# Kernel optimization log

Measured on AMD Instinct MI355X. Metric: run time of the kernel, lower is better.

## Reference

```python
import jax, jax.numpy as jnp
import numpy as np

FACTOR = 5

def setup_inputs() -> dict:
    key = jax.random.key(0)
    k1, k2, k3, k4 = jax.random.split(key, 4)
    B, L, H, D = 4, 4096, 8, 64
    sample_k = min(FACTOR * int(np.ceil(np.log(L))), L)  # 45
    queries = jax.random.normal(k1, (B, L, H, D), jnp.float32)
    keys = jax.random.normal(k2, (B, L, H, D), jnp.float32)
    values = jax.random.normal(k3, (B, L, H, D), jnp.float32)
    # torch.randint(L_K, (L_Q, sample_k)) hoisted here for determinism
    index_sample = jax.random.randint(k4, (L, sample_k), 0, L, dtype=jnp.int32)
    return {"queries": queries, "keys": keys, "values": values,
            "index_sample": index_sample}


def reference(queries, keys, values, index_sample):
    B, L_Q, H, D = queries.shape
    L_K = keys.shape[1]
    # [B,L,H,D] -> [B,H,L,D]
    Q = jnp.transpose(queries, (0, 2, 1, 3))
    K = jnp.transpose(keys, (0, 2, 1, 3))
    V = jnp.transpose(values, (0, 2, 1, 3))

    u = min(FACTOR * int(np.ceil(np.log(L_Q))), L_Q)  # n_top queries

    # --- _prob_QK: sampled QK, sparsity measure, top-u query selection ---
    # K_sample[b,h,q,s,:] = K[b,h,index_sample[q,s],:]
    K_sample = K[:, :, index_sample, :]                        # [B,H,L_Q,Sk,D]
    Q_K_sample = jnp.einsum('bhqd,bhqsd->bhqs', Q, K_sample)   # [B,H,L_Q,Sk]
    M = Q_K_sample.max(axis=-1) - Q_K_sample.sum(axis=-1) / L_K
    _, M_top = jax.lax.top_k(M, u)                             # [B,H,u]

    Q_reduce = jnp.take_along_axis(Q, M_top[..., None], axis=2)  # [B,H,u,D]
    scale = 1.0 / np.sqrt(D).astype(np.float32)
    scores = jnp.einsum('bhud,bhkd->bhuk', Q_reduce, K) * scale  # [B,H,u,L_K]

    # --- masked causal attention on the selected rows (mask_flag=True) ---
    # ProbMask: triu(1) rows gathered at M_top -> mask where col > query pos
    causal_mask = M_top[..., None] < jnp.arange(L_K)             # [B,H,u,L_K]
    scores = jnp.where(causal_mask, -jnp.inf, scores)
    attn = jax.nn.softmax(scores, axis=-1)

    # --- initial context (masked => cumsum of V), scatter top-u updates ---
    context = jnp.cumsum(V, axis=2)                              # [B,H,L_Q,D]
    update = jnp.einsum('bhuk,bhkd->bhud', attn, V)              # [B,H,u,D]
    b_idx = jnp.arange(B)[:, None, None]
    h_idx = jnp.arange(H)[None, :, None]
    context = context.at[b_idx, h_idx, M_top].set(update)
    return context  # [B,H,L_Q,D]
```

## Files before the change

### kernel.cpp

```cpp
#include <hip/hip_runtime.h>
#include <float.h>
#include <math.h>

#define B_ 4
#define L_ 4096
#define H_ 8
#define D_ 64
#define S_ 45
#define KC_ 16
#define KCH_ 256
#define SCALE 0.125f

typedef __attribute__((ext_vector_type(8))) short short8;
typedef __attribute__((ext_vector_type(4))) float float4v;

__device__ __forceinline__ ushort f2bf(float x) {
  unsigned u = __float_as_uint(x);
  return (ushort)((u + 0x7FFFu + ((u >> 16) & 1u)) >> 16);
}

__device__ __forceinline__ int swz_us(int row, int col_b, int rowb, int m) {
  int slot = (col_b >> 4) ^ (row & m);
  return row * (rowb >> 1) + (slot << 3) + ((col_b & 15) >> 1);
}

__device__ __forceinline__ unsigned ordf(float f) {
  unsigned u = __float_as_uint(f);
  return (u & 0x80000000u) ? ~u : (u | 0x80000000u);
}

__global__ __launch_bounds__(256) void kA(
    const float* __restrict__ Q, const float* __restrict__ K,
    const float* __restrict__ V, const int* __restrict__ idxs,
    float* __restrict__ M, float* __restrict__ cs)
{
  int blk = blockIdx.x;
  int grp = blk / 136, within = blk % 136;
  int tid = threadIdx.x;
  int w = tid >> 6, lane = tid & 63;

  if (within >= 128) {
    if (grp >= 64) return;
    int cblk = grp * 8 + (within - 128);
    int bh = cblk >> 4, cg = cblk & 15;
    int b = bh >> 3, h = bh & 7;
    int t = lane & 15, rg = lane >> 4;
    int c = cg * 4 + w;
    int l0 = c * 64;
    const float4* V4 = (const float4*)V;
    float4 acc = make_float4(0.f, 0.f, 0.f, 0.f);
    for (int step = 0; step < 16; ++step) {
      int l = l0 + step * 4 + rg;
      float4 v = V4[((size_t)(b * L_ + l) * H_ + h) * 16 + t];
      acc.x += v.x; acc.y += v.y; acc.z += v.z; acc.w += v.w;
    }
    acc.x += __shfl_xor(acc.x, 16, 64); acc.y += __shfl_xor(acc.y, 16, 64);
    acc.z += __shfl_xor(acc.z, 16, 64); acc.w += __shfl_xor(acc.w, 16, 64);
    acc.x += __shfl_xor(acc.x, 32, 64); acc.y += __shfl_xor(acc.y, 32, 64);
    acc.z += __shfl_xor(acc.z, 32, 64); acc.w += __shfl_xor(acc.w, 32, 64);
    if (rg == 0)
      ((float4*)cs)[((size_t)bh * 64 + c) * 16 + t] = acc;
    return;
  }

  int kblk = grp * 128 + within;
  int phase = kblk >> 13;
  int pblk = kblk & 8191;
  int g = pblk & 7;
  int b = (g >> 2) + phase * 2;
  int hq = g & 3;
  int chunk = pblk >> 3;
  int l = chunk * 4 + w;
  int t31 = lane & 31;
  int half = lane >> 5;

  const float4* qp =
      (const float4*)(Q + ((size_t)(b * L_ + l) * H_ + hq * 2) * D_);
  float4 qv = qp[t31];

  int s = lane < S_ ? lane : S_ - 1;
  int idxall = idxs[l * S_ + s];

  float vmax = -FLT_MAX, vsum = 0.f;
  #pragma unroll
  for (int c = 0; c < 3; ++c) {
    int kidx[6];
    #pragma unroll
    for (int jj = 0; jj < 6; ++jj)
      kidx[jj] = __shfl(idxall, (c * 6 + jj) * 2 + half, 64);
    float4 kv[6];
    #pragma unroll
    for (int jj = 0; jj < 6; ++jj)
      kv[jj] = ((const float4*)(K +
          ((size_t)(b * L_ + kidx[jj]) * H_ + hq * 2) * D_))[t31];
    #pragma unroll
    for (int jj = 0; jj < 6; ++jj) {
      float p = qv.x * kv[jj].x;
      p = fmaf(qv.y, kv[jj].y, p);
      p = fmaf(qv.z, kv[jj].z, p);
      p = fmaf(qv.w, kv[jj].w, p);
      p += __shfl_xor(p, 1, 64);
      p += __shfl_xor(p, 2, 64);
      p += __shfl_xor(p, 4, 64);
      p += __shfl_xor(p, 8, 64);
      vmax = fmaxf(vmax, p);
      vsum += p;
    }
  }
  {
    int kidx[5];
    #pragma unroll
    for (int jj = 0; jj < 5; ++jj) {
      int s2 = (18 + jj) * 2 + half;
      kidx[jj] = __shfl(idxall, s2 > 44 ? 44 : s2, 64);
    }
    float4 kv[5];
    #pragma unroll
    for (int jj = 0; jj < 5; ++jj)
      kv[jj] = ((const float4*)(K +
          ((size_t)(b * L_ + kidx[jj]) * H_ + hq * 2) * D_))[t31];
    #pragma unroll
    for (int jj = 0; jj < 5; ++jj) {
      float p = qv.x * kv[jj].x;
      p = fmaf(qv.y, kv[jj].y, p);
      p = fmaf(qv.z, kv[jj].z, p);
      p = fmaf(qv.w, kv[jj].w, p);
      p += __shfl_xor(p, 1, 64);
      p += __shfl_xor(p, 2, 64);
      p += __shfl_xor(p, 4, 64);
      p += __shfl_xor(p, 8, 64);
      bool dup = (jj == 4) && (half == 1);
      vmax = fmaxf(vmax, p);
      if (!dup) vsum += p;
    }
  }
  vmax = fmaxf(vmax, __shfl_xor(vmax, 32, 64));
  vsum += __shfl_xor(vsum, 32, 64);
  if ((lane & 15) == 0 && half == 0) {
    int h = hq * 2 + (lane >> 4);
    M[(size_t)(b * H_ + h) * L_ + l] = vmax - vsum * (1.0f / L_);
  }
}

__global__ __launch_bounds__(256) void kB(
    const float* __restrict__ M, int* __restrict__ mtop, float* __restrict__ cs)
{
  int blk = blockIdx.x;
  int tid = threadIdx.x;
  if (blk >= 32) {
    int g = (blk - 32) * 256 + tid;
    int bh = g >> 6, d = g & 63;
    float v[64];
    #pragma unroll
    for (int c = 0; c < 64; ++c) v[c] = cs[((size_t)bh * 64 + c) * D_ + d];
    float run = 0.f;
    #pragma unroll
    for (int c = 0; c < 64; ++c) {
      float a = v[c];
      cs[((size_t)bh * 64 + c) * D_ + d] = run;
      run += a;
    }
    return;
  }
  __shared__ unsigned long long cand[4][S_];
  int bh = blk;
  int w = tid >> 6, lane = tid & 63;
  const float* Mp = M + (size_t)bh * L_;
  unsigned long long key[16];
  #pragma unroll
  for (int j = 0; j < 16; ++j) {
    int gi = w * 1024 + j * 64 + lane;
    key[j] = ((unsigned long long)ordf(Mp[gi]) << 32) | (unsigned)(~gi);
  }
  for (int it = 0; it < S_; ++it) {
    unsigned long long loc = key[0];
    #pragma unroll
    for (int j = 1; j < 16; ++j) loc = key[j] > loc ? key[j] : loc;
    unsigned long long best = loc;
    #pragma unroll
    for (int m = 32; m >= 1; m >>= 1) {
      unsigned long long o = __shfl_xor(best, m, 64);
      best = o > best ? o : best;
    }
    if (loc == best) {
      #pragma unroll
      for (int j = 0; j < 16; ++j) if (key[j] == best) key[j] = 0ull;
    }
    if (lane == 0) cand[w][it] = best;
  }
  __syncthreads();
  if (w == 0) {
    unsigned long long k2[3];
    #pragma unroll
    for (int j = 0; j < 3; ++j) {
      int c = j * 64 + lane;
      k2[j] = (c < 4 * S_) ? cand[c / S_][c % S_] : 0ull;
    }
    for (int it = 0; it < S_; ++it) {
      unsigned long long loc = k2[0];
      loc = k2[1] > loc ? k2[1] : loc;
      loc = k2[2] > loc ? k2[2] : loc;
      unsigned long long best = loc;
      #pragma unroll
      for (int m = 32; m >= 1; m >>= 1) {
        unsigned long long o = __shfl_xor(best, m, 64);
        best = o > best ? o : best;
      }
      if (loc == best) {
        #pragma unroll
        for (int j = 0; j < 3; ++j) if (k2[j] == best) k2[j] = 0ull;
      }
      if (lane == 0) mtop[bh * S_ + it] = (int)(~(unsigned)(best & 0xFFFFFFFFu));
    }
  }
}

__global__ __launch_bounds__(256) void kAW(
    const float* __restrict__ Q, const float* __restrict__ K,
    const float* __restrict__ V, const float* __restrict__ cs,
    const int* __restrict__ mtop, float* __restrict__ lpart,
    float* __restrict__ updp, float* __restrict__ out)
{
  __shared__ __align__(16) ushort Ks[256 * 64];
  __shared__ __align__(16) ushort Qs[48 * 64];
  __shared__ __align__(16) ushort Ps[48 * 256];
  __shared__ float lred[4][48];
  __shared__ int   cut[48];
  __shared__ unsigned bits[8];

  int blk = blockIdx.x;
  int grp = blk >> 4, within = blk & 15;
  int tid = threadIdx.x;
  int w = tid >> 6, lane = tid & 63;

  if (within >= 8) {
    int wblk = grp * 8 + (within - 8);
    int bh = wblk >> 4, cg2 = wblk & 15;
    int base = cg2 * 256;
    if (tid < 8) bits[tid] = 0u;
    __syncthreads();
    if (tid < S_) {
      int r = mtop[bh * S_ + tid] - base;
      if ((unsigned)r < 256u) atomicOr(&bits[r >> 5], 1u << (r & 31));
    }
    __syncthreads();

    int b = bh >> 3, h = bh & 7;
    int t = lane & 15, rg = lane >> 4;
    int c = cg2 * 4 + w;
    int l0 = c * 64;
    const float4* V4 = (const float4*)V;
    float4* O4 = (float4*)out;
    float4 carry = ((const float4*)cs)[((size_t)bh * 64 + c) * 16 + t];
    for (int step = 0; step < 16; ++step) {
      int l = l0 + step * 4 + rg;
      float4 v = V4[((size_t)(b * L_ + l) * H_ + h) * 16 + t];
      float4 u;
      u.x = __shfl_up(v.x, 16, 64); u.y = __shfl_up(v.y, 16, 64);
      u.z = __shfl_up(v.z, 16, 64); u.w = __shfl_up(v.w, 16, 64);
      if (rg >= 1) { v.x += u.x; v.y += u.y; v.z += u.z; v.w += u.w; }
      u.x = __shfl_up(v.x, 32, 64); u.y = __shfl_up(v.y, 32, 64);
      u.z = __shfl_up(v.z, 32, 64); u.w = __shfl_up(v.w, 32, 64);
      if (rg >= 2) { v.x += u.x; v.y += u.y; v.z += u.z; v.w += u.w; }
      int wl = l - base;
      if (!((bits[wl >> 5] >> (wl & 31)) & 1u)) {
        float4 o;
        o.x = carry.x + v.x; o.y = carry.y + v.y;
        o.z = carry.z + v.z; o.w = carry.w + v.w;
        O4[((size_t)bh * L_ + l) * 16 + t] = o;
      }
      carry.x += __shfl(v.x, 48 + t, 64); carry.y += __shfl(v.y, 48 + t, 64);
      carry.z += __shfl(v.z, 48 + t, 64); carry.w += __shfl(v.w, 48 + t, 64);
    }
    return;
  }

  int ablk = grp * 8 + within;
  int kc = ablk >> 5;
  int r5 = ablk & 31;
  int bh = ((r5 & 7) << 2) | (r5 >> 3);
  int b = bh >> 3, h = bh & 7;
  int l15 = lane & 15, l4 = lane >> 4;

  float4 vreg[16];
  {
    const float4* vp =
        (const float4*)(V + ((size_t)(b * L_ + kc * KCH_ + tid) * H_ + h) * D_);
    #pragma unroll
    for (int c = 0; c < 16; ++c) vreg[c] = vp[c];
  }

  if (tid < 48) cut[tid] = (tid < S_) ? mtop[bh * S_ + tid] : -1;
  __syncthreads();

  {
    const float4* kp =
        (const float4*)(K + ((size_t)(b * L_ + kc * KCH_ + tid) * H_ + h) * D_);
    #pragma unroll
    for (int c = 0; c < 8; ++c) {
      float4 a = kp[2 * c], bb = kp[2 * c + 1];
      uint4 pk;
      pk.x = f2bf(a.x) | ((unsigned)f2bf(a.y) << 16);
      pk.y = f2bf(a.z) | ((unsigned)f2bf(a.w) << 16);
      pk.z = f2bf(bb.x) | ((unsigned)f2bf(bb.y) << 16);
      pk.w = f2bf(bb.z) | ((unsigned)f2bf(bb.w) << 16);
      *(uint4*)&Ks[swz_us(tid, c * 16, 128, 7)] = pk;
    }
  }
  for (int i = tid; i < 48 * 8; i += 256) {
    int row = i >> 3, c = i & 7;
    uint4 pk = make_uint4(0, 0, 0, 0);
    if (row < S_) {
      const float4* qp =
          (const float4*)(Q + ((size_t)(b * L_ + cut[row]) * H_ + h) * D_);
      float4 a = qp[2 * c], bb = qp[2 * c + 1];
      pk.x = f2bf(a.x) | ((unsigned)f2bf(a.y) << 16);
      pk.y = f2bf(a.z) | ((unsigned)f2bf(a.w) << 16);
      pk.z = f2bf(bb.x) | ((unsigned)f2bf(bb.y) << 16);
      pk.w = f2bf(bb.z) | ((unsigned)f2bf(bb.w) << 16);
    }
    *(uint4*)&Qs[swz_us(row, c * 16, 128, 7)] = pk;
  }
  __syncthreads();

  float4v accS[3][4];
  #pragma unroll
  for (int mt = 0; mt < 3; ++mt)
    #pragma unroll
    for (int nt = 0; nt < 4; ++nt)
      accS[mt][nt] = (float4v){0.f, 0.f, 0.f, 0.f};
  #pragma unroll
  for (int ks = 0; ks < 2; ++ks) {
    short8 afr[3];
    #pragma unroll
    for (int mt = 0; mt < 3; ++mt)
      afr[mt] = *(const short8*)&Qs[swz_us(mt * 16 + l15, ks * 64 + l4 * 16, 128, 7)];
    #pragma unroll
    for (int nt = 0; nt < 4; ++nt) {
      short8 bfr = *(const short8*)
          &Ks[swz_us(w * 64 + nt * 16 + l15, ks * 64 + l4 * 16, 128, 7)];
      #pragma unroll
      for (int mt = 0; mt < 3; ++mt)
        accS[mt][nt] = __builtin_amdgcn_mfma_f32_16x16x32_bf16(
            afr[mt], bfr, accS[mt][nt], 0, 0, 0);
    }
  }

  #pragma unroll
  for (int mt = 0; mt < 3; ++mt) {
    #pragma unroll
    for (int j = 0; j < 4; ++j) {
      int row = mt * 16 + l4 * 4 + j;
      int ct = cut[row];
      float rs = 0.f;
      #pragma unroll
      for (int nt = 0; nt < 4; ++nt) {
        int col = w * 64 + nt * 16 + l15;
        int kg = kc * KCH_ + col;
        float e = (kg <= ct) ? __expf(accS[mt][nt][j] * SCALE) : 0.f;
        rs += e;
        Ps[swz_us(row, col * 2, 512, 15)] = f2bf(e);
      }
      rs += __shfl_xor(rs, 1, 64);
      rs += __shfl_xor(rs, 2, 64);
      rs += __shfl_xor(rs, 4, 64);
      rs += __shfl_xor(rs, 8, 64);
      if (l15 == 0) lred[w][row] = rs;
    }
  }
  __syncthreads();

  if (tid < S_)
    lpart[((size_t)(bh * KC_ + kc)) * S_ + tid] =
        lred[0][tid] + lred[1][tid] + lred[2][tid] + lred[3][tid];

  #pragma unroll
  for (int c = 0; c < 16; ++c) {
    float4 v = vreg[c];
    int d0 = c * 4;
    Ks[swz_us(d0 + 0, tid * 2, 512, 15)] = f2bf(v.x);
    Ks[swz_us(d0 + 1, tid * 2, 512, 15)] = f2bf(v.y);
    Ks[swz_us(d0 + 2, tid * 2, 512, 15)] = f2bf(v.z);
    Ks[swz_us(d0 + 3, tid * 2, 512, 15)] = f2bf(v.w);
  }
  __syncthreads();

  float4v accU[3];
  #pragma unroll
  for (int i = 0; i < 3; ++i) accU[i] = (float4v){0.f, 0.f, 0.f, 0.f};
  #pragma unroll
  for (int ks = 0; ks < 8; ++ks) {
    #pragma unroll
    for (int i = 0; i < 3; ++i) {
      int pi = w * 3 + i, mt = pi >> 2, nt = pi & 3;
      short8 afr = *(const short8*)
          &Ps[swz_us(mt * 16 + l15, ks * 64 + l4 * 16, 512, 15)];
      short8 bfr = *(const short8*)
          &Ks[swz_us(nt * 16 + l15, ks * 64 + l4 * 16, 512, 15)];
      accU[i] = __builtin_amdgcn_mfma_f32_16x16x32_bf16(afr, bfr, accU[i], 0, 0, 0);
    }
  }
  float* up = updp + ((size_t)(bh * KC_ + kc)) * (S_ * D_);
  #pragma unroll
  for (int i = 0; i < 3; ++i) {
    int pi = w * 3 + i, mt = pi >> 2, nt = pi & 3;
    #pragma unroll
    for (int j = 0; j < 4; ++j) {
      int row = mt * 16 + l4 * 4 + j;
      if (row < S_) up[row * D_ + nt * 16 + l15] = accU[i][j];
    }
  }
}

__global__ __launch_bounds__(256) void kFin(
    const float* __restrict__ lpart, const float* __restrict__ updp,
    const int* __restrict__ mtop, float* __restrict__ out)
{
  __shared__ float linv[S_];
  __shared__ int   mt[S_];
  int bh = blockIdx.x;
  int tid = threadIdx.x;
  if (tid < S_) {
    float l = 0.f;
    for (int kc = 0; kc < KC_; ++kc) l += lpart[(size_t)(bh * KC_ + kc) * S_ + tid];
    linv[tid] = 1.0f / l;
    mt[tid] = mtop[bh * S_ + tid];
  }
  __syncthreads();
  for (int i = tid; i < S_ * D_; i += 256) {
    int r = i >> 6, d = i & 63;
    float u = 0.f;
    for (int kc = 0; kc < KC_; ++kc) u += updp[((size_t)(bh * KC_ + kc)) * (S_ * D_) + i];
    out[((size_t)bh * L_ + mt[r]) * D_ + d] = u * linv[r];
  }
}

extern "C" void kernel_launch(void* const* d_in, const int* in_sizes, int n_in,
                              void* d_out, int out_size, void* d_ws, size_t ws_size,
                              hipStream_t stream) {
  const float* Q = (const float*)d_in[0];
  const float* K = (const float*)d_in[1];
  const float* V = (const float*)d_in[2];
  const int*   I = (const int*)d_in[3];
  float* out = (float*)d_out;
  float* ws = (float*)d_ws;

  float* M     = ws;
  float* cs    = ws + 131072;
  float* lpart = ws + 262144;
  float* updp  = ws + 262144 + 23040;
  int*   mtop  = (int*)(ws + 262144 + 23040 + 1474560);

  kA<<<128 * 136, 256, 0, stream>>>(Q, K, V, I, M, cs);
  kB<<<40, 256, 0, stream>>>(M, mtop, cs);
  kAW<<<64 * 16, 256, 0, stream>>>(Q, K, V, cs, mtop, lpart, updp, out);
  kFin<<<B_ * H_, 256, 0, stream>>>(lpart, updp, mtop, out);
}
```

Before: 187.9 us.

## Fuse four kernels into two using atomic flags and last-block finalization

Cuts the launch sequence from four kernels to two. The cumsum output write moves into kA, where blocks spin on per-head counters until the chunk sums are ready. Top-k selection and attention run in one kernel kTail: attention blocks spin on a per-head flag set by the top-k blocks, and the last attention block per head performs the final reduction and scatter. This removes launch gaps and lets phases overlap, but it adds spin-wait loops that rely on the producer blocks being scheduled first, an extra memset, and a risk of deadlock if that scheduling order is not guaranteed.

```diff
diff --git a/kernel.cpp b/kernel.cpp
--- a/kernel.cpp
+++ b/kernel.cpp
@@ -32,7 +32,8 @@
 __global__ __launch_bounds__(256) void kA(
     const float* __restrict__ Q, const float* __restrict__ K,
     const float* __restrict__ V, const int* __restrict__ idxs,
-    float* __restrict__ M, float* __restrict__ cs)
+    float* __restrict__ M, float* __restrict__ cs,
+    float* __restrict__ out, int* __restrict__ ctr)
 {
   int blk = blockIdx.x;
   int grp = blk / 136, within = blk % 136;
@@ -40,26 +41,69 @@
   int w = tid >> 6, lane = tid & 63;
 
   if (within >= 128) {
-    if (grp >= 64) return;
-    int cblk = grp * 8 + (within - 128);
-    int bh = cblk >> 4, cg = cblk & 15;
+    if (grp < 64) {
+      int cblk = grp * 8 + (within - 128);
+      int bh = cblk >> 4, cg = cblk & 15;
+      int b = bh >> 3, h = bh & 7;
+      int t = lane & 15, rg = lane >> 4;
+      int c = cg * 4 + w;
+      int l0 = c * 64;
+      const float4* V4 = (const float4*)V;
+      float4 acc = make_float4(0.f, 0.f, 0.f, 0.f);
+      for (int step = 0; step < 16; ++step) {
+        int l = l0 + step * 4 + rg;
+        float4 v = V4[((size_t)(b * L_ + l) * H_ + h) * 16 + t];
+        acc.x += v.x; acc.y += v.y; acc.z += v.z; acc.w += v.w;
+      }
+      acc.x += __shfl_xor(acc.x, 16, 64); acc.y += __shfl_xor(acc.y, 16, 64);
+      acc.z += __shfl_xor(acc.z, 16, 64); acc.w += __shfl_xor(acc.w, 16, 64);
+      acc.x += __shfl_xor(acc.x, 32, 64); acc.y += __shfl_xor(acc.y, 32, 64);
+      acc.z += __shfl_xor(acc.z, 32, 64); acc.w += __shfl_xor(acc.w, 32, 64);
+      if (rg == 0)
+        ((float4*)cs)[((size_t)bh * 64 + c) * 16 + t] = acc;
+      __syncthreads();
+      if (tid == 0) {
+        __threadfence();
+        atomicAdd(&ctr[bh], 1);
+      }
+      return;
+    }
+    int wblk = (grp - 64) * 8 + (within - 128);
+    int bh = wblk >> 4, cg2 = wblk & 15;
+    if (tid == 0) {
+      while (atomicAdd(&ctr[bh], 0) < 16) { }
+    }
+    __syncthreads();
+    __threadfence();
     int b = bh >> 3, h = bh & 7;
     int t = lane & 15, rg = lane >> 4;
-    int c = cg * 4 + w;
+    int c = cg2 * 4 + w;
     int l0 = c * 64;
+    const float4* cs4 = (const float4*)cs;
+    float4 carry = make_float4(0.f, 0.f, 0.f, 0.f);
+    for (int cc = 0; cc < c; ++cc) {
+      float4 x = cs4[((size_t)bh * 64 + cc) * 16 + t];
+      carry.x += x.x; carry.y += x.y; carry.z += x.z; carry.w += x.w;
+    }
     const float4* V4 = (const float4*)V;
-    float4 acc = make_float4(0.f, 0.f, 0.f, 0.f);
+    float4* O4 = (float4*)out;
     for (int step = 0; step < 16; ++step) {
       int l = l0 + step * 4 + rg;
       float4 v = V4[((size_t)(b * L_ + l) * H_ + h) * 16 + t];
-      acc.x += v.x; acc.y += v.y; acc.z += v.z; acc.w += v.w;
-    }
-    acc.x += __shfl_xor(acc.x, 16, 64); acc.y += __shfl_xor(acc.y, 16, 64);
-    acc.z += __shfl_xor(acc.z, 16, 64); acc.w += __shfl_xor(acc.w, 16, 64);
-    acc.x += __shfl_xor(acc.x, 32, 64); acc.y += __shfl_xor(acc.y, 32, 64);
-    acc.z += __shfl_xor(acc.z, 32, 64); acc.w += __shfl_xor(acc.w, 32, 64);
-    if (rg == 0)
-      ((float4*)cs)[((size_t)bh * 64 + c) * 16 + t] = acc;
+      float4 u;
+      u.x = __shfl_up(v.x, 16, 64); u.y = __shfl_up(v.y, 16, 64);
+      u.z = __shfl_up(v.z, 16, 64); u.w = __shfl_up(v.w, 16, 64);
+      if (rg >= 1) { v.x += u.x; v.y += u.y; v.z += u.z; v.w += u.w; }
+      u.x = __shfl_up(v.x, 32, 64); u.y = __shfl_up(v.y, 32, 64);
+      u.z = __shfl_up(v.z, 32, 64); u.w = __shfl_up(v.w, 32, 64);
+      if (rg >= 2) { v.x += u.x; v.y += u.y; v.z += u.z; v.w += u.w; }
+      float4 o;
+      o.x = carry.x + v.x; o.y = carry.y + v.y;
+      o.z = carry.z + v.z; o.w = carry.w + v.w;
+      O4[((size_t)bh * L_ + l) * 16 + t] = o;
+      carry.x += __shfl(v.x, 48 + t, 64); carry.y += __shfl(v.y, 48 + t, 64);
+      carry.z += __shfl(v.z, 48 + t, 64); carry.w += __shfl(v.w, 48 + t, 64);
+    }
     return;
   }
 
@@ -142,140 +186,83 @@
   }
 }
 
-__global__ __launch_bounds__(256) void kB(
-    const float* __restrict__ M, int* __restrict__ mtop, float* __restrict__ cs)
-{
-  int blk = blockIdx.x;
-  int tid = threadIdx.x;
-  if (blk >= 32) {
-    int g = (blk - 32) * 256 + tid;
-    int bh = g >> 6, d = g & 63;
-    float v[64];
-    #pragma unroll
-    for (int c = 0; c < 64; ++c) v[c] = cs[((size_t)bh * 64 + c) * D_ + d];
-    float run = 0.f;
-    #pragma unroll
-    for (int c = 0; c < 64; ++c) {
-      float a = v[c];
-      cs[((size_t)bh * 64 + c) * D_ + d] = run;
-      run += a;
-    }
-    return;
-  }
-  __shared__ unsigned long long cand[4][S_];
-  int bh = blk;
-  int w = tid >> 6, lane = tid & 63;
-  const float* Mp = M + (size_t)bh * L_;
-  unsigned long long key[16];
-  #pragma unroll
-  for (int j = 0; j < 16; ++j) {
-    int gi = w * 1024 + j * 64 + lane;
-    key[j] = ((unsigned long long)ordf(Mp[gi]) << 32) | (unsigned)(~gi);
-  }
-  for (int it = 0; it < S_; ++it) {
-    unsigned long long loc = key[0];
-    #pragma unroll
-    for (int j = 1; j < 16; ++j) loc = key[j] > loc ? key[j] : loc;
-    unsigned long long best = loc;
-    #pragma unroll
-    for (int m = 32; m >= 1; m >>= 1) {
-      unsigned long long o = __shfl_xor(best, m, 64);
-      best = o > best ? o : best;
-    }
-    if (loc == best) {
-      #pragma unroll
-      for (int j = 0; j < 16; ++j) if (key[j] == best) key[j] = 0ull;
-    }
-    if (lane == 0) cand[w][it] = best;
-  }
-  __syncthreads();
-  if (w == 0) {
-    unsigned long long k2[3];
-    #pragma unroll
-    for (int j = 0; j < 3; ++j) {
-      int c = j * 64 + lane;
-      k2[j] = (c < 4 * S_) ? cand[c / S_][c % S_] : 0ull;
-    }
-    for (int it = 0; it < S_; ++it) {
-      unsigned long long loc = k2[0];
-      loc = k2[1] > loc ? k2[1] : loc;
-      loc = k2[2] > loc ? k2[2] : loc;
-      unsigned long long best = loc;
-      #pragma unroll
-      for (int m = 32; m >= 1; m >>= 1) {
-        unsigned long long o = __shfl_xor(best, m, 64);
-        best = o > best ? o : best;
-      }
-      if (loc == best) {
-        #pragma unroll
-        for (int j = 0; j < 3; ++j) if (k2[j] == best) k2[j] = 0ull;
-      }
-      if (lane == 0) mtop[bh * S_ + it] = (int)(~(unsigned)(best & 0xFFFFFFFFu));
-    }
-  }
-}
-
-__global__ __launch_bounds__(256) void kAW(
+__global__ __launch_bounds__(256) void kTail(
     const float* __restrict__ Q, const float* __restrict__ K,
-    const float* __restrict__ V, const float* __restrict__ cs,
-    const int* __restrict__ mtop, float* __restrict__ lpart,
-    float* __restrict__ updp, float* __restrict__ out)
+    const float* __restrict__ V, const float* __restrict__ M,
+    int* __restrict__ mtop, float* __restrict__ lpart,
+    float* __restrict__ updp, float* __restrict__ out,
+    int* __restrict__ flag, int* __restrict__ ctr2)
 {
   __shared__ __align__(16) ushort Ks[256 * 64];
   __shared__ __align__(16) ushort Qs[48 * 64];
   __shared__ __align__(16) ushort Ps[48 * 256];
   __shared__ float lred[4][48];
   __shared__ int   cut[48];
-  __shared__ unsigned bits[8];
+  __shared__ int   doFin;
 
   int blk = blockIdx.x;
-  int grp = blk >> 4, within = blk & 15;
   int tid = threadIdx.x;
   int w = tid >> 6, lane = tid & 63;
 
-  if (within >= 8) {
-    int wblk = grp * 8 + (within - 8);
-    int bh = wblk >> 4, cg2 = wblk & 15;
-    int base = cg2 * 256;
-    if (tid < 8) bits[tid] = 0u;
+  if (blk < 32) {
+    unsigned long long (*cand)[S_] = (unsigned long long (*)[S_])Ps;
+    int bh = blk;
+    const float* Mp = M + (size_t)bh * L_;
+    unsigned long long key[16];
+    #pragma unroll
+    for (int j = 0; j < 16; ++j) {
+      int gi = w * 1024 + j * 64 + lane;
+      key[j] = ((unsigned long long)ordf(Mp[gi]) << 32) | (unsigned)(~gi);
+    }
+    for (int it = 0; it < S_; ++it) {
+      unsigned long long loc = key[0];
+      #pragma unroll
+      for (int j = 1; j < 16; ++j) loc = key[j] > loc ? key[j] : loc;
+      unsigned long long best = loc;
+      #pragma unroll
+      for (int m = 32; m >= 1; m >>= 1) {
+        unsigned long long o = __shfl_xor(best, m, 64);
+        best = o > best ? o : best;
+      }
+      if (loc == best) {
+        #pragma unroll
+        for (int j = 0; j < 16; ++j) if (key[j] == best) key[j] = 0ull;
+      }
+      if (lane == 0) cand[w][it] = best;
+    }
     __syncthreads();
-    if (tid < S_) {
-      int r = mtop[bh * S_ + tid] - base;
-      if ((unsigned)r < 256u) atomicOr(&bits[r >> 5], 1u << (r & 31));
-    }
-    __syncthreads();
-
-    int b = bh >> 3, h = bh & 7;
-    int t = lane & 15, rg = lane >> 4;
-    int c = cg2 * 4 + w;
-    int l0 = c * 64;
-    const float4* V4 = (const float4*)V;
-    float4* O4 = (float4*)out;
-    float4 carry = ((const float4*)cs)[((size_t)bh * 64 + c) * 16 + t];
-    for (int step = 0; step < 16; ++step) {
-      int l = l0 + step * 4 + rg;
-      float4 v = V4[((size_t)(b * L_ + l) * H_ + h) * 16 + t];
-      float4 u;
-      u.x = __shfl_up(v.x, 16, 64); u.y = __shfl_up(v.y, 16, 64);
-      u.z = __shfl_up(v.z, 16, 64); u.w = __shfl_up(v.w, 16, 64);
-      if (rg >= 1) { v.x += u.x; v.y += u.y; v.z += u.z; v.w += u.w; }
-      u.x = __shfl_up(v.x, 32, 64); u.y = __shfl_up(v.y, 32, 64);
-      u.z = __shfl_up(v.z, 32, 64); u.w = __shfl_up(v.w, 32, 64);
-      if (rg >= 2) { v.x += u.x; v.y += u.y; v.z += u.z; v.w += u.w; }
-      int wl = l - base;
-      if (!((bits[wl >> 5] >> (wl & 31)) & 1u)) {
-        float4 o;
-        o.x = carry.x + v.x; o.y = carry.y + v.y;
-        o.z = carry.z + v.z; o.w = carry.w + v.w;
-        O4[((size_t)bh * L_ + l) * 16 + t] = o;
-      }
-      carry.x += __shfl(v.x, 48 + t, 64); carry.y += __shfl(v.y, 48 + t, 64);
-      carry.z += __shfl(v.z, 48 + t, 64); carry.w += __shfl(v.w, 48 + t, 64);
+    if (w == 0) {
+      unsigned long long k2[3];
+      #pragma unroll
+      for (int j = 0; j < 3; ++j) {
+        int c = j * 64 + lane;
+        k2[j] = (c < 4 * S_) ? cand[c / S_][c % S_] : 0ull;
+      }
+      for (int it = 0; it < S_; ++it) {
+        unsigned long long loc = k2[0];
+        loc = k2[1] > loc ? k2[1] : loc;
+        loc = k2[2] > loc ? k2[2] : loc;
+        unsigned long long best = loc;
+        #pragma unroll
+        for (int m = 32; m >= 1; m >>= 1) {
+          unsigned long long o = __shfl_xor(best, m, 64);
+          best = o > best ? o : best;
+        }
+        if (loc == best) {
+          #pragma unroll
+          for (int j = 0; j < 3; ++j) if (k2[j] == best) k2[j] = 0ull;
+        }
+        if (lane == 0) mtop[bh * S_ + it] = (int)(~(unsigned)(best & 0xFFFFFFFFu));
+      }
+      if (lane == 0) {
+        __threadfence();
+        atomicExch(&flag[bh], 1);
+      }
     }
     return;
   }
 
-  int ablk = grp * 8 + within;
+  int ablk = blk - 32;
   int kc = ablk >> 5;
   int r5 = ablk & 31;
   int bh = ((r5 & 7) << 2) | (r5 >> 3);
@@ -289,10 +276,6 @@
     #pragma unroll
     for (int c = 0; c < 16; ++c) vreg[c] = vp[c];
   }
-
-  if (tid < 48) cut[tid] = (tid < S_) ? mtop[bh * S_ + tid] : -1;
-  __syncthreads();
-
   {
     const float4* kp =
         (const float4*)(K + ((size_t)(b * L_ + kc * KCH_ + tid) * H_ + h) * D_);
@@ -307,6 +290,14 @@
       *(uint4*)&Ks[swz_us(tid, c * 16, 128, 7)] = pk;
     }
   }
+  if (tid == 0) {
+    while (atomicAdd(&flag[bh], 0) == 0) { }
+  }
+  __syncthreads();
+  __threadfence();
+
+  if (tid < 48) cut[tid] = (tid < S_) ? mtop[bh * S_ + tid] : -1;
+  __syncthreads();
   for (int i = tid; i < 48 * 8; i += 256) {
     int row = i >> 3, c = i & 7;
     uint4 pk = make_uint4(0, 0, 0, 0);
@@ -410,28 +401,31 @@
       if (row < S_) up[row * D_ + nt * 16 + l15] = accU[i][j];
     }
   }
-}
-
-__global__ __launch_bounds__(256) void kFin(
-    const float* __restrict__ lpart, const float* __restrict__ updp,
-    const int* __restrict__ mtop, float* __restrict__ out)
-{
-  __shared__ float linv[S_];
-  __shared__ int   mt[S_];
-  int bh = blockIdx.x;
-  int tid = threadIdx.x;
-  if (tid < S_) {
-    float l = 0.f;
-    for (int kc = 0; kc < KC_; ++kc) l += lpart[(size_t)(bh * KC_ + kc) * S_ + tid];
-    linv[tid] = 1.0f / l;
-    mt[tid] = mtop[bh * S_ + tid];
-  }
-  __syncthreads();
-  for (int i = tid; i < S_ * D_; i += 256) {
-    int r = i >> 6, d = i & 63;
-    float u = 0.f;
-    for (int kc = 0; kc < KC_; ++kc) u += updp[((size_t)(bh * KC_ + kc)) * (S_ * D_) + i];
-    out[((size_t)bh * L_ + mt[r]) * D_ + d] = u * linv[r];
+
+  __syncthreads();
+  if (tid == 0) {
+    __threadfence();
+    int old = atomicAdd(&ctr2[bh], 1);
+    doFin = (old == KC_ - 1) ? 1 : 0;
+  }
+  __syncthreads();
+  if (doFin) {
+    __threadfence();
+    float* linvp = lred[0];
+    if (tid < S_) {
+      float l = 0.f;
+      for (int kcc = 0; kcc < KC_; ++kcc)
+        l += lpart[(size_t)(bh * KC_ + kcc) * S_ + tid];
+      linvp[tid] = 1.0f / l;
+    }
+    __syncthreads();
+    for (int i = tid; i < S_ * D_; i += 256) {
+      int r = i >> 6, d = i & 63;
+      float u = 0.f;
+      for (int kcc = 0; kcc < KC_; ++kcc)
+        u += updp[((size_t)(bh * KC_ + kcc)) * (S_ * D_) + i];
+      out[((size_t)bh * L_ + cut[r]) * D_ + d] = u * linvp[r];
+    }
   }
 }
 
@@ -450,9 +444,11 @@
   float* lpart = ws + 262144;
   float* updp  = ws + 262144 + 23040;
   int*   mtop  = (int*)(ws + 262144 + 23040 + 1474560);
-
-  kA<<<128 * 136, 256, 0, stream>>>(Q, K, V, I, M, cs);
-  kB<<<40, 256, 0, stream>>>(M, mtop, cs);
-  kAW<<<64 * 16, 256, 0, stream>>>(Q, K, V, cs, mtop, lpart, updp, out);
-  kFin<<<B_ * H_, 256, 0, stream>>>(lpart, updp, mtop, out);
-}
+  int*   ctr   = mtop + 1440;
+  int*   flag  = ctr + 32;
+  int*   ctr2  = flag + 32;
+
+  hipMemsetAsync(ctr, 0, 96 * sizeof(int), stream);
+  kA<<<128 * 136, 256, 0, stream>>>(Q, K, V, I, M, cs, out, ctr);
+  kTail<<<544, 256, 0, stream>>>(Q, K, V, M, mtop, lpart, updp, out, flag, ctr2);
+}
```

New measurement: 307.4 us. 1.64x slower.
